# Kernel optimization log

Measured on AMD Instinct MI355X. Metric: run time of the kernel, lower is better.

## Reference

```python
import jax, jax.numpy as jnp
import numpy as np

B, N, H, R = 128, 512, 256, 3
VIRTUAL_DECAY = 0.7


def _build_tree():
    # Deterministic random recursive tree: parent[i] ~ U[0, i)
    rng = np.random.default_rng(0)
    parent = np.zeros(N, np.int64)
    for i in range(1, N):
        parent[i] = rng.integers(0, i)
    depth = np.zeros(N, np.int64)
    for i in range(1, N):
        depth[i] = depth[parent[i]] + 1
    rel_edge = rng.integers(0, R, N)          # relation type of edge (parent -> i)
    virtual = rng.random(N) < 0.1
    children = [[] for _ in range(N)]
    for i in range(1, N):
        children[parent[i]].append(i)
    # Group internal nodes by depth (deepest first == valid post-order batching),
    # pad ragged child lists per level.
    levels = []
    for d in range(int(depth.max()), -1, -1):
        nodes = [n for n in range(N) if depth[n] == d and len(children[n]) > 0]
        if not nodes:
            continue
        cmax = max(len(children[n]) for n in nodes)
        M = len(nodes)
        cidx = np.zeros((M, cmax), np.int64)
        cmask = np.zeros((M, cmax), np.float32)
        crel = np.zeros((M, cmax), np.int64)
        cvirt = np.zeros((M, cmax), bool)
        for m, n in enumerate(nodes):
            ch = children[n]
            k = len(ch)
            cidx[m, :k] = ch
            cmask[m, :k] = 1.0
            crel[m, :k] = rel_edge[ch]
            cvirt[m, :k] = virtual[ch]
        levels.append((jnp.array(nodes), jnp.array(cidx), jnp.array(cmask),
                       jnp.array(crel), jnp.array(cvirt)))
    return levels

LEVELS = _build_tree()


def _forward(node_features, W_enc, b_enc, rel_emb, W_i, b_i, W_o, b_o, W_u, b_u,
             W_f, b_f, w_attn, b_attn):
    h = node_features @ W_enc + b_enc            # (B, N, H) node_encoder
    c = jnp.zeros_like(h)
    for node_ids, cidx, cmask, crel, cvirt in LEVELS:
        x = h[:, node_ids]                       # (B, M, H) input_vec (== encoded feats)
        ch_h = h[:, cidx]                        # (B, M, C, H)
        ch_c = c[:, cidx]
        # virtual-node decay + padding mask
        decay = jnp.where(cvirt, VIRTUAL_DECAY, 1.0).astype(h.dtype) * cmask  # (M, C)
        ch_h = ch_h * decay[None, :, :, None]
        ch_c = ch_c * decay[None, :, :, None]
        # relation-aware attention over children
        re = rel_emb[crel]                       # (M, C, H)
        scores = jnp.einsum('bmch,h->bmc', re[None] + ch_h, w_attn) + b_attn[0]
        scores = jnp.where(cmask[None] > 0, scores, -1e9)
        attw = jax.nn.softmax(scores, axis=-1)   # (B, M, C)
        h_sum = jnp.einsum('bmc,bmch->bmh', attw, ch_h)
        # per-relation forget transform (note: original applies NO sigmoid here)
        f = jnp.zeros_like(ch_h)
        for r in range(R):
            fr = jnp.einsum('bmch,hk->bmck', ch_h, W_f[r]) + b_f[r]
            f = f + fr * (crel == r).astype(h.dtype)[None, :, :, None]
        c_sum = jnp.sum(f * ch_c, axis=2)        # (B, M, H); padded ch_c is 0
        comb = jnp.concatenate([x, h_sum], axis=-1)  # (B, M, 2H)
        i_g = jax.nn.sigmoid(comb @ W_i + b_i)
        o_g = jax.nn.sigmoid(comb @ W_o + b_o)
        u_g = jnp.tanh(comb @ W_u + b_u)
        c_new = i_g * u_g + c_sum
        h_new = o_g * jnp.tanh(c_new)
        h = h.at[:, node_ids].set(h_new)
        c = c.at[:, node_ids].set(c_new)
    return h[:, 0]                               # pooling == 'root' (root = 0)


def setup_inputs() -> dict:
    key = jax.random.key(0)
    ks = jax.random.split(key, 8)
    s = 0.05
    f32 = jnp.float32
    return {
        'node_features': jax.random.normal(ks[0], (B, N, H), f32),
        'W_enc': jax.random.normal(ks[1], (H, H), f32) * s,
        'b_enc': jnp.full((H,), 0.1, f32),
        'rel_emb': jax.random.normal(ks[2], (R, H), f32) * s,
        'W_i': jax.random.normal(ks[3], (2 * H, H), f32) * s,
        'b_i': jnp.full((H,), 0.1, f32),
        'W_o': jax.random.normal(ks[4], (2 * H, H), f32) * s,
        'b_o': jnp.full((H,), 0.1, f32),
        'W_u': jax.random.normal(ks[5], (2 * H, H), f32) * s,
        'b_u': jnp.full((H,), 0.1, f32),
        'W_f': jax.random.normal(ks[6], (R, H, H), f32) * s,
        'b_f': jnp.full((R, H), 0.1, f32),
        'w_attn': jax.random.normal(ks[7], (H,), f32) * s,
        'b_attn': jnp.full((1,), 0.1, f32),
    }


def reference(node_features, W_enc, b_enc, rel_emb, W_i, b_i, W_o, b_o, W_u, b_u,
              W_f, b_f, w_attn, b_attn):
    return _forward(node_features, W_enc, b_enc, rel_emb, W_i, b_i, W_o, b_o,
                    W_u, b_u, W_f, b_f, w_attn, b_attn)
```

## Files before the change

kernel.cpp:

```cpp
#include <hip/hip_runtime.h>
#include <stdint.h>
#include <string.h>
#include <math.h>

#define NB 128
#define NN 512
#define NH 256
#define NR 3

typedef __attribute__((ext_vector_type(8))) short bh8;
typedef __attribute__((ext_vector_type(4))) float f32x4;

struct Pcg {
  __uint128_t state, inc;
  bool has32; uint32_t buf32;
};

static const __uint128_t PCG_MULT =
    (((__uint128_t)2549297995355413924ULL) << 64) | 4865540595714422341ULL;

static inline uint64_t pcg_next64(Pcg& s) {
  s.state = s.state * PCG_MULT + s.inc;
  uint64_t hi = (uint64_t)(s.state >> 64), lo = (uint64_t)s.state;
  uint64_t x = hi ^ lo;
  unsigned rot = (unsigned)(s.state >> 122) & 63u;
  return (x >> rot) | (x << ((64u - rot) & 63u));
}
static inline uint32_t pcg_next32(Pcg& s) {
  if (s.has32) { s.has32 = false; return s.buf32; }
  uint64_t n = pcg_next64(s);
  s.has32 = true; s.buf32 = (uint32_t)(n >> 32);
  return (uint32_t)n;
}
static inline uint64_t pcg_bounded(Pcg& s, uint64_t high) {
  uint64_t rng = high - 1;
  if (rng == 0) return 0;
  uint32_t rng_excl = (uint32_t)rng + 1u;
  uint64_t m = (uint64_t)pcg_next32(s) * (uint64_t)rng_excl;
  uint32_t leftover = (uint32_t)m;
  if (leftover < rng_excl) {
    uint32_t threshold = (uint32_t)((0xFFFFFFFFu - (uint32_t)rng) % rng_excl);
    while (leftover < threshold) {
      m = (uint64_t)pcg_next32(s) * (uint64_t)rng_excl;
      leftover = (uint32_t)m;
    }
  }
  return m >> 32;
}
static inline double pcg_double(Pcg& s) {
  return (double)(pcg_next64(s) >> 11) * (1.0 / 9007199254740992.0);
}

static void pcg_seed0(Pcg& s) {
  uint32_t pool[4];
  uint32_t hc = 0x43b0d7e5u;
  auto hashmix = [&hc](uint32_t v) -> uint32_t {
    v ^= hc; hc *= 0x931e8875u; v *= hc; v ^= v >> 16; return v;
  };
  auto mix = [](uint32_t x, uint32_t y) -> uint32_t {
    uint32_t r = 0xca01f9ddu * x - 0x4973f715u * y; r ^= r >> 16; return r;
  };
  for (int i = 0; i < 4; i++) pool[i] = hashmix(0u);
  for (int src = 0; src < 4; src++)
    for (int dst = 0; dst < 4; dst++)
      if (src != dst) pool[dst] = mix(pool[dst], hashmix(pool[src]));
  uint32_t gs[8]; uint32_t hb = 0x8b51f9ddu;
  for (int i = 0; i < 8; i++) {
    uint32_t dv = pool[i & 3];
    dv ^= hb; hb *= 0x58f38dedu; dv *= hb; dv ^= dv >> 16;
    gs[i] = dv;
  }
  uint64_t w0 = (uint64_t)gs[0] | ((uint64_t)gs[1] << 32);
  uint64_t w1 = (uint64_t)gs[2] | ((uint64_t)gs[3] << 32);
  uint64_t w2 = (uint64_t)gs[4] | ((uint64_t)gs[5] << 32);
  uint64_t w3 = (uint64_t)gs[6] | ((uint64_t)gs[7] << 32);
  __uint128_t initstate = (((__uint128_t)w0) << 64) | w1;
  __uint128_t initseq   = (((__uint128_t)w2) << 64) | w3;
  s.state = 0;
  s.inc = (initseq << 1) | 1;
  s.state = s.state * PCG_MULT + s.inc;
  s.state += initstate;
  s.state = s.state * PCG_MULT + s.inc;
  s.has32 = false; s.buf32 = 0;
}

struct TreeMeta {
  int nodes[512];
  int cstart[512];
  int ccount[512];
  int echild[512];
  int erel[512];
  float edecay[512];
  int cechild[512];
  int cepar[512];
  int cerel[512];
  float cedec[512];
  int cens[513];
};
struct HostTree {
  TreeMeta meta;
  int n_levels;
  int level_off[520];
  int level_M[520];
};

static void build_tree_host(HostTree& T) {
  Pcg st; pcg_seed0(st);
  int parent[NN], depth[NN], rel[NN];
  unsigned char virt[NN];
  parent[0] = 0; depth[0] = 0;
  for (int i = 1; i < NN; i++) parent[i] = (int)pcg_bounded(st, (uint64_t)i);
  for (int i = 1; i < NN; i++) depth[i] = depth[parent[i]] + 1;
  for (int i = 0; i < NN; i++) rel[i] = (int)pcg_bounded(st, (uint64_t)NR);
  for (int i = 0; i < NN; i++) virt[i] = (pcg_double(st) < 0.1) ? 1 : 0;

  int childcnt[NN]; memset(childcnt, 0, sizeof(childcnt));
  for (int i = 1; i < NN; i++) childcnt[parent[i]]++;
  int maxd = 0;
  for (int i = 0; i < NN; i++) if (depth[i] > maxd) maxd = depth[i];

  int ni = 0, ne = 0, nec = 0;
  T.n_levels = 0;
  for (int d = maxd; d >= 0; d--) {
    int mstart = ni;
    for (int n = 0; n < NN; n++) {
      if (depth[n] == d && childcnt[n] > 0) {
        T.meta.nodes[ni] = n;
        T.meta.cstart[ni] = ne;
        T.meta.ccount[ni] = childcnt[n];
        T.meta.cens[ni] = nec;
        for (int i2 = 1; i2 < NN; i2++) {
          if (parent[i2] == n) {
            T.meta.echild[ne] = i2;
            T.meta.erel[ne] = rel[i2];
            T.meta.edecay[ne] = virt[i2] ? 0.7f : 1.0f;
            ne++;
            if (childcnt[i2] > 0) {
              T.meta.cechild[nec] = i2;
              T.meta.cepar[nec] = n;
              T.meta.cerel[nec] = rel[i2];
              T.meta.cedec[nec] = virt[i2] ? 0.7f : 1.0f;
              nec++;
            }
          }
        }
        ni++;
      }
    }
    if (ni > mstart) {
      T.level_off[T.n_levels] = mstart;
      T.level_M[T.n_levels] = ni - mstart;
      T.n_levels++;
    }
  }
  T.meta.cens[ni] = nec;
}

__device__ __forceinline__ uint16_t f2bf(float f) {
  uint32_t u = __float_as_uint(f);
  return (uint16_t)((u + 0x7fffu + ((u >> 16) & 1u)) >> 16);
}
__device__ __forceinline__ float bf2f(uint16_t b) {
  return __uint_as_float(((uint32_t)b) << 16);
}
__device__ __forceinline__ float sigm(float x) {
  return 1.f / (1.f + expf(-x));
}

__device__ __forceinline__ void stage_bf16(uint16_t* __restrict__ sm,
    const uint16_t* __restrict__ src, int stride, int rows) {
  const int chunks = rows << 3;
  for (int cch = threadIdx.x; cch < chunks; cch += 256) {
    const int row = cch >> 3, k = (cch & 7) << 3;
    uint4 v = *(const uint4*)(src + (size_t)row * stride + k);
    *(uint4*)(sm + (((row << 6) + k) ^ ((row & 7) << 3))) = v;
  }
}
__device__ __forceinline__ void stage_f32(uint16_t* __restrict__ sm,
    const float* __restrict__ src, int stride, int rows) {
  const int chunks = rows << 3;
  for (int cch = threadIdx.x; cch < chunks; cch += 256) {
    const int row = cch >> 3, k = (cch & 7) << 3;
    const float* p = src + (size_t)row * stride + k;
    float4 a = *(const float4*)p, b = *(const float4*)(p + 4);
    uint4 w;
    w.x = (uint32_t)f2bf(a.x) | ((uint32_t)f2bf(a.y) << 16);
    w.y = (uint32_t)f2bf(a.z) | ((uint32_t)f2bf(a.w) << 16);
    w.z = (uint32_t)f2bf(b.x) | ((uint32_t)f2bf(b.y) << 16);
    w.w = (uint32_t)f2bf(b.z) | ((uint32_t)f2bf(b.w) << 16);
    *(uint4*)(sm + (((row << 6) + k) ^ ((row & 7) << 3))) = w;
  }
}
__device__ __forceinline__ bh8 fld(const uint16_t* __restrict__ sm, int row, int k) {
  return *(const bh8*)(sm + (((row << 6) + k) ^ ((row & 7) << 3)));
}

#define LDROW(BUF, CH) do { \
    const uint4* p_ = (const uint4*)(hbase + (size_t)(CH) * NH); \
    BUF[0]=p_[0]; BUF[1]=p_[1]; BUF[2]=p_[2]; BUF[3]=p_[3]; \
    BUF[4]=p_[4]; BUF[5]=p_[5]; BUF[6]=p_[6]; BUF[7]=p_[7]; } while (0)
#define ACCROW(BUF, W) do { const float w_ = (W); \
    _Pragma("unroll") for (int v_ = 0; v_ < 8; v_++) { \
      const uint16_t* pe_ = (const uint16_t*)&BUF[v_]; \
      _Pragma("unroll") for (int q_ = 0; q_ < 8; q_++) \
        hs[v_*8+q_] = fmaf(bf2f(pe_[q_]), w_, hs[v_*8+q_]); } } while (0)

__global__ __launch_bounds__(256) void k_prep(const float* __restrict__ We,
    const float* __restrict__ Wf, const float* __restrict__ Wi,
    const float* __restrict__ Wo, const float* __restrict__ Wu,
    uint16_t* __restrict__ WeT, uint16_t* __restrict__ WfT,
    uint16_t* __restrict__ WgT) {
  const int i = blockIdx.x * 256 + threadIdx.x;
  if (i < 65536) {
    const int n = i >> 8, k = i & 255;
    WeT[i] = f2bf(We[k * 256 + n]);
  }
  const int i2 = i - 65536;
  if (i2 >= 0 && i2 < 196608) {
    const int r = i2 >> 16, rem = i2 & 65535, n = rem >> 8, k = rem & 255;
    WfT[i2] = f2bf(Wf[r * 65536 + k * 256 + n]);
  }
  const int i3 = i - 262144;
  if (i3 >= 0 && i3 < 393216) {
    const int g = i3 >> 17, rem = i3 & 131071, n = rem >> 9, k = rem & 511;
    const float* S = (g == 0) ? Wi : (g == 1) ? Wo : Wu;
    WgT[i3] = f2bf(S[k * 256 + n]);
  }
}

__global__ __launch_bounds__(256) void k_enc(const float* __restrict__ nf,
    const uint16_t* __restrict__ WeT, const float* __restrict__ b_enc,
    uint16_t* __restrict__ h_bf, uint16_t* __restrict__ x_enc) {
  __shared__ __align__(16) uint16_t smA[128 * 64];
  __shared__ __align__(16) uint16_t smB[128 * 64];
  const int bm = blockIdx.x * 128, bn = blockIdx.y * 128;
  const int tid = threadIdx.x, wid = tid >> 6, lane = tid & 63;
  const int wr = wid >> 1, wc2 = wid & 1, lr = lane & 15, lk = (lane >> 4) << 3;
  f32x4 acc[4][4] = {};
  for (int k0 = 0; k0 < 256; k0 += 64) {
    __syncthreads();
    stage_f32(smA, nf + (size_t)bm * NH + k0, NH, 128);
    stage_bf16(smB, WeT + (size_t)bn * 256 + k0, 256, 128);
    __syncthreads();
#pragma unroll
    for (int ks = 0; ks < 2; ks++) {
      bh8 af[4], bfr[4];
#pragma unroll
      for (int i = 0; i < 4; i++) af[i] = fld(smA, wr * 64 + i * 16 + lr, ks * 32 + lk);
#pragma unroll
      for (int j = 0; j < 4; j++) bfr[j] = fld(smB, wc2 * 64 + j * 16 + lr, ks * 32 + lk);
#pragma unroll
      for (int i = 0; i < 4; i++)
#pragma unroll
        for (int j = 0; j < 4; j++)
          acc[i][j] = __builtin_amdgcn_mfma_f32_16x16x32_bf16(af[i], bfr[j], acc[i][j], 0, 0, 0);
    }
  }
#pragma unroll
  for (int i = 0; i < 4; i++) {
#pragma unroll
    for (int j = 0; j < 4; j++) {
      const int col = bn + wc2 * 64 + j * 16 + (lane & 15);
      const float be = b_enc[col];
#pragma unroll
      for (int r = 0; r < 4; r++) {
        const int row = bm + wr * 64 + i * 16 + (lane >> 4) * 4 + r;
        const uint16_t hv = f2bf(acc[i][j][r] + be);
        h_bf[(size_t)row * NH + col] = hv;
        x_enc[(size_t)row * NH + col] = hv;
      }
    }
  }
}

__global__ __launch_bounds__(256) void k_sv0(const uint16_t* __restrict__ h_bf,
    const float* __restrict__ w_attn, float* __restrict__ svp) {
  const int idx = blockIdx.x * 256 + threadIdx.x;
  const int g = idx & 15;
  const size_t row = (size_t)(idx >> 4);
  const uint16_t* hp = h_bf + row * NH + g * 16;
  uint4 p0 = *(const uint4*)hp, p1 = *(const uint4*)(hp + 8);
  const uint16_t* e0 = (const uint16_t*)&p0;
  const uint16_t* e1 = (const uint16_t*)&p1;
  float s = 0.f;
#pragma unroll
  for (int u = 0; u < 8; u++) s = fmaf(bf2f(e0[u]), w_attn[g * 16 + u], s);
#pragma unroll
  for (int u = 0; u < 8; u++) s = fmaf(bf2f(e1[u]), w_attn[g * 16 + 8 + u], s);
  svp[idx] = s;
}

__global__ __launch_bounds__(256) void k_ac(
    const uint16_t* __restrict__ h_bf, float* c, const float* __restrict__ svp,
    const uint16_t* __restrict__ WfT, const float* __restrict__ b_f,
    const float* __restrict__ rel_emb, const float* __restrict__ w_attn,
    const float* __restrict__ b_attn, uint16_t* __restrict__ comb,
    const TreeMeta* __restrict__ tm, int nb, int M, int ce0) {
  const int tid = threadIdx.x, wid = tid >> 6, lane = tid & 63;
  const int bx = blockIdx.x;

  if (bx >= 2 * M) {
    const int e8 = bx - 2 * M;
    const int ce = ce0 + (e8 >> 3);
    const int sub = e8 & 7;
    const int b0 = (sub >> 2) * 64, cslice = (sub & 3) * 64;
    const int ch = tm->cechild[ce], par = tm->cepar[ce], rel = tm->cerel[ce];
    const float dec = tm->cedec[ce];
    const int lr2 = lane & 15, hi4 = lane >> 4, lk = hi4 << 3;
    const int colw = cslice + wid * 16 + lr2;
    const uint16_t* Wr = WfT + (size_t)rel * 65536 + (size_t)colw * 256;
    f32x4 facc[4] = {};
#pragma unroll
    for (int k0 = 0; k0 < 8; k0++) {
      const int kk = k0 * 32 + lk;
      bh8 af[4];
#pragma unroll
      for (int i = 0; i < 4; i++)
        af[i] = *(const bh8*)(h_bf + ((size_t)(b0 + i * 16 + lr2) * NN + ch) * NH + kk);
      const bh8 bq = *(const bh8*)(Wr + kk);
#pragma unroll
      for (int i = 0; i < 4; i++)
        facc[i] = __builtin_amdgcn_mfma_f32_16x16x32_bf16(af[i], bq, facc[i], 0, 0, 0);
    }
    const float bfv = b_f[rel * NH + colw];
#pragma unroll
    for (int i = 0; i < 4; i++) {
#pragma unroll
      for (int r = 0; r < 4; r++) {
        const int brow = b0 + i * 16 + hi4 * 4 + r;
        const float cch = c[((size_t)brow * NN + ch) * NH + colw];
        atomicAdd(&c[((size_t)brow * NN + par) * NH + colw],
                  (dec * facc[i][r] + bfv) * (dec * cch));
      }
    }
  } else {
    __shared__ float sc[64 * 65];
    __shared__ float sRE[3];
    __shared__ int chl[64]; __shared__ int rll[64]; __shared__ float dcl[64];
    const int mloc = bx >> 1, b0 = (bx & 1) * 64;
    const int gi = nb + mloc;
    const int cs = tm->cstart[gi], cc = tm->ccount[gi];

    if (tid < cc) {
      chl[tid] = tm->echild[cs + tid];
      rll[tid] = tm->erel[cs + tid];
      dcl[tid] = tm->edecay[cs + tid];
    }
    if (wid < 3) {
      float p = 0.f;
#pragma unroll
      for (int i = 0; i < 4; i++) p += rel_emb[wid * NH + lane + 64 * i] * w_attn[lane + 64 * i];
#pragma unroll
      for (int off = 32; off; off >>= 1) p += __shfl_down(p, off);
      if (lane == 0) sRE[wid] = p;
    }
    __syncthreads();

    const float ba = b_attn[0];
    if (tid < 64) {
      const float* svpb = svp + (size_t)(b0 + tid) * NN * 16;
      for (int e = 0; e < cc; e++) {
        const float4* p = (const float4*)(svpb + chl[e] * 16);
        float4 a = p[0], b2 = p[1], c2 = p[2], d2 = p[3];
        float s = ((a.x + a.y) + (a.z + a.w)) + ((b2.x + b2.y) + (b2.z + b2.w)) +
                  ((c2.x + c2.y) + (c2.z + c2.w)) + ((d2.x + d2.y) + (d2.z + d2.w));
        sc[tid * 65 + e] = sRE[rll[e]] + dcl[e] * s + ba;
      }
      float mx = -1e30f;
      for (int e = 0; e < cc; e++) mx = fmaxf(mx, sc[tid * 65 + e]);
      float ss = 0.f;
      for (int e = 0; e < cc; e++) ss += expf(sc[tid * 65 + e] - mx);
      const float inv = 1.0f / ss;
      for (int e = 0; e < cc; e++) sc[tid * 65 + e] = expf(sc[tid * 65 + e] - mx) * inv * dcl[e];
    }
    __syncthreads();

    const int sb = tid >> 2, sq = tid & 3;
    float hs[64];
#pragma unroll
    for (int v = 0; v < 64; v++) hs[v] = 0.f;
    const uint16_t* hbase = h_bf + (size_t)(b0 + sb) * NN * NH + sq * 64;
    uint4 bufA[8], bufB[8];
    LDROW(bufA, chl[0]);
    int e = 0;
    for (; e + 2 <= cc; e += 2) {
      LDROW(bufB, chl[e + 1]);
      ACCROW(bufA, sc[sb * 65 + e]);
      if (e + 2 < cc) LDROW(bufA, chl[e + 2]);
      ACCROW(bufB, sc[sb * 65 + e + 1]);
    }
    if (e < cc) ACCROW(bufA, sc[sb * 65 + e]);
    uint16_t* cb = comb + ((size_t)(mloc * 128 + b0 + sb)) * 256 + sq * 64;
#pragma unroll
    for (int v = 0; v < 8; v++) {
      uint4 w;
      w.x = (uint32_t)f2bf(hs[8 * v + 0]) | ((uint32_t)f2bf(hs[8 * v + 1]) << 16);
      w.y = (uint32_t)f2bf(hs[8 * v + 2]) | ((uint32_t)f2bf(hs[8 * v + 3]) << 16);
      w.z = (uint32_t)f2bf(hs[8 * v + 4]) | ((uint32_t)f2bf(hs[8 * v + 5]) << 16);
      w.w = (uint32_t)f2bf(hs[8 * v + 6]) | ((uint32_t)f2bf(hs[8 * v + 7]) << 16);
      *(uint4*)(cb + v * 8) = w;
    }
  }
}

__global__ __launch_bounds__(256) void k_gates(
    uint16_t* h_bf, float* c, float* __restrict__ svp,
    const uint16_t* __restrict__ x_enc, const uint16_t* __restrict__ comb,
    const uint16_t* __restrict__ WgT,
    const float* __restrict__ b_i, const float* __restrict__ b_o,
    const float* __restrict__ b_u, const float* __restrict__ w_attn,
    float* __restrict__ out, const TreeMeta* __restrict__ tm, int nb) {
  const int bx = blockIdx.x, mloc = bx >> 1, b0 = (bx & 1) * 64;
  const int cslice = blockIdx.y * 64;
  const int gi = nb + mloc;
  const int nd = tm->nodes[gi];
  const int tid = threadIdx.x, wid = tid >> 6, lane = tid & 63;
  const int lr2 = lane & 15, hi4 = lane >> 4, lk = hi4 << 3;
  const int colw = cslice + wid * 16 + lr2;

  f32x4 ga[3][4] = {};
#pragma unroll
  for (int k32 = 0; k32 < 16; k32++) {
    const int kk = k32 * 32 + lk;
    bh8 af[4], bq[3];
    if (k32 < 8) {
#pragma unroll
      for (int i = 0; i < 4; i++)
        af[i] = *(const bh8*)(x_enc + ((size_t)(b0 + i * 16 + lr2) * NN + nd) * NH + kk);
    } else {
#pragma unroll
      for (int i = 0; i < 4; i++)
        af[i] = *(const bh8*)(comb + ((size_t)(mloc * 128 + b0 + i * 16 + lr2)) * 256 + (kk - 256));
    }
#pragma unroll
    for (int g = 0; g < 3; g++)
      bq[g] = *(const bh8*)(WgT + ((size_t)g << 17) + (size_t)colw * 512 + kk);
#pragma unroll
    for (int g = 0; g < 3; g++)
#pragma unroll
      for (int i = 0; i < 4; i++)
        ga[g][i] = __builtin_amdgcn_mfma_f32_16x16x32_bf16(af[i], bq[g], ga[g][i], 0, 0, 0);
  }

  const float bi_ = b_i[colw], bo_ = b_o[colw], bu_ = b_u[colw];
  const float wac = w_attn[colw];
#pragma unroll
  for (int i = 0; i < 4; i++) {
#pragma unroll
    for (int r = 0; r < 4; r++) {
      const int brow = b0 + i * 16 + hi4 * 4 + r;
      const size_t idx = ((size_t)brow * NN + nd) * NH + colw;
      const float ig = sigm(ga[0][i][r] + bi_);
      const float og = sigm(ga[1][i][r] + bo_);
      const float ug = tanhf(ga[2][i][r] + bu_);
      const float cn = fmaf(ig, ug, c[idx]);
      c[idx] = cn;
      const float hn = og * tanhf(cn);
      h_bf[idx] = f2bf(hn);
      if (nd == 0) out[(size_t)brow * NH + colw] = hn;
      float pv = hn * wac;
      pv += __shfl_xor(pv, 1); pv += __shfl_xor(pv, 2);
      pv += __shfl_xor(pv, 4); pv += __shfl_xor(pv, 8);
      if (lr2 == 0) svp[((size_t)brow * NN + nd) * 16 + (cslice >> 4) + wid] = pv;
    }
  }
}

extern "C" void kernel_launch(void* const* d_in, const int* in_sizes, int n_in,
                              void* d_out, int out_size, void* d_ws, size_t ws_size,
                              hipStream_t stream) {
  (void)in_sizes; (void)n_in; (void)out_size; (void)ws_size;
  const float* nf      = (const float*)d_in[0];
  const float* W_enc   = (const float*)d_in[1];
  const float* b_enc   = (const float*)d_in[2];
  const float* rel_emb = (const float*)d_in[3];
  const float* W_i     = (const float*)d_in[4];
  const float* b_i     = (const float*)d_in[5];
  const float* W_o     = (const float*)d_in[6];
  const float* b_o     = (const float*)d_in[7];
  const float* W_u     = (const float*)d_in[8];
  const float* b_u     = (const float*)d_in[9];
  const float* W_f     = (const float*)d_in[10];
  const float* b_f     = (const float*)d_in[11];
  const float* w_attn  = (const float*)d_in[12];
  const float* b_attn  = (const float*)d_in[13];
  float* out = (float*)d_out;

  static HostTree T;
  build_tree_host(T);

  char* ws = (char*)d_ws;
  const size_t OFF_HBF  = 32768;
  const size_t SZ_HBF   = (size_t)NB * NN * NH * 2;
  const size_t OFF_XE   = OFF_HBF + SZ_HBF;
  const size_t OFF_WET  = OFF_XE + SZ_HBF;
  const size_t OFF_WFT  = OFF_WET + 131072;
  const size_t OFF_WGT  = OFF_WFT + 393216;
  const size_t OFF_C    = OFF_WGT + 786432;
  const size_t SZ_C     = (size_t)NB * NN * NH * 4;
  const size_t OFF_SVP  = OFF_C + SZ_C;
  const size_t OFF_COMB = OFF_SVP + (size_t)NB * NN * 16 * 4;

  TreeMeta* dm = (TreeMeta*)ws;
  uint16_t* h_bf = (uint16_t*)(ws + OFF_HBF);
  uint16_t* x_enc = (uint16_t*)(ws + OFF_XE);
  uint16_t* WeT = (uint16_t*)(ws + OFF_WET);
  uint16_t* WfT = (uint16_t*)(ws + OFF_WFT);
  uint16_t* WgT = (uint16_t*)(ws + OFF_WGT);
  float* c = (float*)(ws + OFF_C);
  float* svp = (float*)(ws + OFF_SVP);
  uint16_t* comb = (uint16_t*)(ws + OFF_COMB);

  hipMemcpyAsync(dm, &T.meta, sizeof(TreeMeta), hipMemcpyHostToDevice, stream);
  hipMemsetAsync(c, 0, SZ_C, stream);

  k_prep<<<2560, 256, 0, stream>>>(W_enc, W_f, W_i, W_o, W_u, WeT, WfT, WgT);
  k_enc<<<dim3((NB * NN) / 128, 2), 256, 0, stream>>>(nf, WeT, b_enc, h_bf, x_enc);
  k_sv0<<<dim3((NB * NN * 16) / 256), 256, 0, stream>>>(h_bf, w_attn, svp);

  for (int l = 0; l < T.n_levels; l++) {
    const int Mfull = T.level_M[l];
    for (int c0 = 0; c0 < Mfull; c0 += 128) {
      const int Mc = (Mfull - c0) < 128 ? (Mfull - c0) : 128;
      const int nb = T.level_off[l] + c0;
      const int ce0 = T.meta.cens[nb];
      const int nCE = T.meta.cens[nb + Mc] - ce0;
      k_ac<<<dim3(2 * Mc + 8 * nCE), 256, 0, stream>>>(h_bf, c, svp, WfT, b_f,
          rel_emb, w_attn, b_attn, comb, dm, nb, Mc, ce0);
      k_gates<<<dim3(2 * Mc, 4), 256, 0, stream>>>(h_bf, c, svp, x_enc, comb,
          WgT, b_i, b_o, b_u, w_attn, out, dm, nb);
    }
  }
}
```

Before: 692.7 us.

## Fuse attention score partials into encoder and drop duplicate x_enc buffer

```diff
diff --git a/kernel.cpp b/kernel.cpp
--- a/kernel.cpp
+++ b/kernel.cpp
@@ -230,7 +230,8 @@
 
 __global__ __launch_bounds__(256) void k_enc(const float* __restrict__ nf,
     const uint16_t* __restrict__ WeT, const float* __restrict__ b_enc,
-    uint16_t* __restrict__ h_bf, uint16_t* __restrict__ x_enc) {
+    const float* __restrict__ w_attn,
+    uint16_t* __restrict__ h_bf, float* __restrict__ svp) {
   __shared__ __align__(16) uint16_t smA[128 * 64];
   __shared__ __align__(16) uint16_t smB[128 * 64];
   const int bm = blockIdx.x * 128, bn = blockIdx.y * 128;
@@ -260,34 +261,21 @@
   for (int i = 0; i < 4; i++) {
 #pragma unroll
     for (int j = 0; j < 4; j++) {
-      const int col = bn + wc2 * 64 + j * 16 + (lane & 15);
+      const int col = bn + wc2 * 64 + j * 16 + lr;
       const float be = b_enc[col];
+      const float wac = w_attn[col];
 #pragma unroll
       for (int r = 0; r < 4; r++) {
         const int row = bm + wr * 64 + i * 16 + (lane >> 4) * 4 + r;
-        const uint16_t hv = f2bf(acc[i][j][r] + be);
-        h_bf[(size_t)row * NH + col] = hv;
-        x_enc[(size_t)row * NH + col] = hv;
+        const float hv = bf2f(f2bf(acc[i][j][r] + be));
+        h_bf[(size_t)row * NH + col] = f2bf(hv);
+        float pv = hv * wac;
+        pv += __shfl_xor(pv, 1); pv += __shfl_xor(pv, 2);
+        pv += __shfl_xor(pv, 4); pv += __shfl_xor(pv, 8);
+        if (lr == 0) svp[(size_t)row * 16 + (col >> 4)] = pv;
       }
     }
   }
-}
-
-__global__ __launch_bounds__(256) void k_sv0(const uint16_t* __restrict__ h_bf,
-    const float* __restrict__ w_attn, float* __restrict__ svp) {
-  const int idx = blockIdx.x * 256 + threadIdx.x;
-  const int g = idx & 15;
-  const size_t row = (size_t)(idx >> 4);
-  const uint16_t* hp = h_bf + row * NH + g * 16;
-  uint4 p0 = *(const uint4*)hp, p1 = *(const uint4*)(hp + 8);
-  const uint16_t* e0 = (const uint16_t*)&p0;
-  const uint16_t* e1 = (const uint16_t*)&p1;
-  float s = 0.f;
-#pragma unroll
-  for (int u = 0; u < 8; u++) s = fmaf(bf2f(e0[u]), w_attn[g * 16 + u], s);
-#pragma unroll
-  for (int u = 0; u < 8; u++) s = fmaf(bf2f(e1[u]), w_attn[g * 16 + 8 + u], s);
-  svp[idx] = s;
 }
 
 __global__ __launch_bounds__(256) void k_ac(
@@ -339,7 +327,7 @@
     __shared__ int chl[64]; __shared__ int rll[64]; __shared__ float dcl[64];
     const int mloc = bx >> 1, b0 = (bx & 1) * 64;
     const int gi = nb + mloc;
-    const int cs = tm->cstart[gi], cc = tm->ccount[gi];
+    const int nd = tm->nodes[gi], cs = tm->cstart[gi], cc = tm->ccount[gi];
 
     if (tid < cc) {
       chl[tid] = tm->echild[cs + tid];
@@ -375,6 +363,12 @@
     }
     __syncthreads();
 
+    for (int idx = tid; idx < 64 * 32; idx += 256) {
+      const int crow = idx >> 5, c8 = (idx & 31) << 3;
+      uint4 v = *(const uint4*)(h_bf + ((size_t)(b0 + crow) * NN + nd) * NH + c8);
+      *(uint4*)(comb + ((size_t)(mloc * 128 + b0 + crow)) * 512 + c8) = v;
+    }
+
     const int sb = tid >> 2, sq = tid & 3;
     float hs[64];
 #pragma unroll
@@ -390,7 +384,7 @@
       ACCROW(bufB, sc[sb * 65 + e + 1]);
     }
     if (e < cc) ACCROW(bufA, sc[sb * 65 + e]);
-    uint16_t* cb = comb + ((size_t)(mloc * 128 + b0 + sb)) * 256 + sq * 64;
+    uint16_t* cb = comb + ((size_t)(mloc * 128 + b0 + sb)) * 512 + 256 + sq * 64;
 #pragma unroll
     for (int v = 0; v < 8; v++) {
       uint4 w;
@@ -405,8 +399,7 @@
 
 __global__ __launch_bounds__(256) void k_gates(
     uint16_t* h_bf, float* c, float* __restrict__ svp,
-    const uint16_t* __restrict__ x_enc, const uint16_t* __restrict__ comb,
-    const uint16_t* __restrict__ WgT,
+    const uint16_t* __restrict__ comb, const uint16_t* __restrict__ WgT,
     const float* __restrict__ b_i, const float* __restrict__ b_o,
     const float* __restrict__ b_u, const float* __restrict__ w_attn,
     float* __restrict__ out, const TreeMeta* __restrict__ tm, int nb) {
@@ -423,15 +416,9 @@
   for (int k32 = 0; k32 < 16; k32++) {
     const int kk = k32 * 32 + lk;
     bh8 af[4], bq[3];
-    if (k32 < 8) {
-#pragma unroll
-      for (int i = 0; i < 4; i++)
-        af[i] = *(const bh8*)(x_enc + ((size_t)(b0 + i * 16 + lr2) * NN + nd) * NH + kk);
-    } else {
-#pragma unroll
-      for (int i = 0; i < 4; i++)
-        af[i] = *(const bh8*)(comb + ((size_t)(mloc * 128 + b0 + i * 16 + lr2)) * 256 + (kk - 256));
-    }
+#pragma unroll
+    for (int i = 0; i < 4; i++)
+      af[i] = *(const bh8*)(comb + ((size_t)(mloc * 128 + b0 + i * 16 + lr2)) * 512 + kk);
 #pragma unroll
     for (int g = 0; g < 3; g++)
       bq[g] = *(const bh8*)(WgT + ((size_t)g << 17) + (size_t)colw * 512 + kk);
@@ -492,8 +479,7 @@
   char* ws = (char*)d_ws;
   const size_t OFF_HBF  = 32768;
   const size_t SZ_HBF   = (size_t)NB * NN * NH * 2;
-  const size_t OFF_XE   = OFF_HBF + SZ_HBF;
-  const size_t OFF_WET  = OFF_XE + SZ_HBF;
+  const size_t OFF_WET  = OFF_HBF + SZ_HBF;
   const size_t OFF_WFT  = OFF_WET + 131072;
   const size_t OFF_WGT  = OFF_WFT + 393216;
   const size_t OFF_C    = OFF_WGT + 786432;
@@ -503,7 +489,6 @@
 
   TreeMeta* dm = (TreeMeta*)ws;
   uint16_t* h_bf = (uint16_t*)(ws + OFF_HBF);
-  uint16_t* x_enc = (uint16_t*)(ws + OFF_XE);
   uint16_t* WeT = (uint16_t*)(ws + OFF_WET);
   uint16_t* WfT = (uint16_t*)(ws + OFF_WFT);
   uint16_t* WgT = (uint16_t*)(ws + OFF_WGT);
@@ -515,8 +500,8 @@
   hipMemsetAsync(c, 0, SZ_C, stream);
 
   k_prep<<<2560, 256, 0, stream>>>(W_enc, W_f, W_i, W_o, W_u, WeT, WfT, WgT);
-  k_enc<<<dim3((NB * NN) / 128, 2), 256, 0, stream>>>(nf, WeT, b_enc, h_bf, x_enc);
-  k_sv0<<<dim3((NB * NN * 16) / 256), 256, 0, stream>>>(h_bf, w_attn, svp);
+  k_enc<<<dim3((NB * NN) / 128, 2), 256, 0, stream>>>(nf, WeT, b_enc, w_attn,
+                                                      h_bf, svp);
 
   for (int l = 0; l < T.n_levels; l++) {
     const int Mfull = T.level_M[l];
@@ -527,7 +512,7 @@
       const int nCE = T.meta.cens[nb + Mc] - ce0;
       k_ac<<<dim3(2 * Mc + 8 * nCE), 256, 0, stream>>>(h_bf, c, svp, WfT, b_f,
           rel_emb, w_attn, b_attn, comb, dm, nb, Mc, ce0);
-      k_gates<<<dim3(2 * Mc, 4), 256, 0, stream>>>(h_bf, c, svp, x_enc, comb,
+      k_gates<<<dim3(2 * Mc, 4), 256, 0, stream>>>(h_bf, c, svp, comb,
           WgT, b_i, b_o, b_u, w_attn, out, dm, nb);
     }
   }
```

Measured after the change: 716.3 us. +3.4%, slower.
